# Performance work log

Hardware: AMD Instinct MI355X
Metric: run time of the kernel (lower is better)

Reference implementation:

```python
import jax, jax.numpy as jnp
import numpy as np

B, T, DIM, HEADS, DH = 4, 2048, 1024, 16, 64  # dh = dim // heads


def setup_inputs() -> dict:
    key = jax.random.key(0)
    k1, k2, k3 = jax.random.split(key, 3)
    x = jax.random.normal(k1, (B, T, DIM), dtype=jnp.float32)
    # nn.Linear weights, stored as [in, out] for x @ W convention
    W_qkv = jax.random.normal(k2, (DIM, 3 * HEADS * DH), dtype=jnp.float32) * (DIM ** -0.5)
    W_o = jax.random.normal(k3, (HEADS * DH, DIM), dtype=jnp.float32) * ((HEADS * DH) ** -0.5)
    return {"x": x, "W_qkv": W_qkv, "W_o": W_o}


def reference(x, W_qkv, W_o):
    b, t, _ = x.shape
    qkv = x @ W_qkv  # [b, t, 3*h*dh]
    # einops 'b t (d k h) -> k b h t d' with k=3, h=HEADS: fused axis splits as (dh, 3, h)
    qkv = qkv.reshape(b, t, DH, 3, HEADS)
    qkv = jnp.transpose(qkv, (3, 0, 4, 1, 2))  # [3, b, h, t, dh]
    q, k, v = qkv[0], qkv[1], qkv[2]
    scale = DH ** -0.5
    scores = jnp.einsum('bhid,bhjd->bhij', q, k) * scale  # [b, h, t, t]
    attn = jax.nn.softmax(scores, axis=-1)
    out = jnp.einsum('bhij,bhjd->bhid', attn, v)  # [b, h, t, dh]
    out = jnp.transpose(out, (0, 2, 1, 3)).reshape(b, t, HEADS * DH)  # 'b h t d -> b t (h d)'
    return out @ W_o
```

## Files before the change

kernel.cpp:

```cpp
#include <hip/hip_runtime.h>

typedef __bf16 bf16;
typedef __bf16 bf16x4 __attribute__((ext_vector_type(4)));
typedef __bf16 bf16x8 __attribute__((ext_vector_type(8)));
typedef float  f32x4  __attribute__((ext_vector_type(4)));
typedef unsigned int u32;
typedef unsigned int u32x2 __attribute__((ext_vector_type(2)));
typedef unsigned int u32x4 __attribute__((ext_vector_type(4)));

#define LOG2E 1.44269504088896340736f
#define EXP_SC (0.125f * LOG2E)

#if __has_builtin(__builtin_amdgcn_exp2f)
#define EXP2F(x) __builtin_amdgcn_exp2f(x)
#else
#define EXP2F(x) __builtin_exp2f(x)
#endif

__device__ __forceinline__ u32 pk_bf16(float lo, float hi) {
  u32 a = __float_as_uint(lo) + 0x8000u;
  u32 b = __float_as_uint(hi) + 0x8000u;
  return __builtin_amdgcn_perm(b, a, 0x07060302);
}
__device__ __forceinline__ unsigned short bf16r(float x) {
  return (unsigned short)((__float_as_uint(x) + 0x8000u) >> 16);
}

__device__ __forceinline__ void async_ld16(void* lds, const void* g) {
  __builtin_amdgcn_global_load_lds(
      (const __attribute__((address_space(1))) void*)(g),
      (__attribute__((address_space(3))) void*)(lds),
      16, 0, 0);
}

__global__ void convert_x(const float* __restrict__ x, bf16* __restrict__ xb) {
  int i = blockIdx.x * 256 + threadIdx.x;
  float4 v = ((const float4*)x)[i];
  u32x2 o = { pk_bf16(v.x, v.y), pk_bf16(v.z, v.w) };
  *(u32x2*)(xb + (size_t)i * 4) = o;
}

__global__ void prep_wqkv(const float* __restrict__ W, bf16* __restrict__ WT) {
  __shared__ float s[4 * 3072];
  const int k0 = blockIdx.x * 4;
  for (int i = threadIdx.x; i < 3072; i += 256) {
    int r = i / 768, c = (i - r * 768) * 4;
    *(float4*)(s + r * 3072 + c) = *(const float4*)(W + (size_t)(k0 + r) * 3072 + c);
  }
  __syncthreads();
  for (int n = threadIdx.x; n < 3072; n += 256) {
    int d = n & 63, h = (n >> 6) & 15, wch = n >> 10;
    int on = d * 48 + wch * 16 + h;
    u32x2 v = { pk_bf16(s[0 * 3072 + on], s[1 * 3072 + on]),
                pk_bf16(s[2 * 3072 + on], s[3 * 3072 + on]) };
    *(u32x2*)(WT + (size_t)n * 1024 + k0) = v;
  }
}

__global__ void prep_wo(const float* __restrict__ W, bf16* __restrict__ WT) {
  __shared__ float s[8 * 1024];
  const int k0 = blockIdx.x * 8;
  for (int i = threadIdx.x; i < 2048; i += 256) {
    int r = i >> 8, c = (i & 255) * 4;
    *(float4*)(s + r * 1024 + c) = *(const float4*)(W + (size_t)(k0 + r) * 1024 + c);
  }
  __syncthreads();
  for (int n = threadIdx.x; n < 1024; n += 256) {
    u32x4 v = { pk_bf16(s[0 * 1024 + n], s[1 * 1024 + n]),
                pk_bf16(s[2 * 1024 + n], s[3 * 1024 + n]),
                pk_bf16(s[4 * 1024 + n], s[5 * 1024 + n]),
                pk_bf16(s[6 * 1024 + n], s[7 * 1024 + n]) };
    *(u32x4*)(WT + (size_t)n * 1024 + k0) = v;
  }
}

template <int MODE>
__launch_bounds__(256, 2)
__global__ void gemm_bt(const bf16* __restrict__ A, const bf16* __restrict__ BT,
                        float* __restrict__ C, int N,
                        bf16* __restrict__ Qb, bf16* __restrict__ Kb, bf16* __restrict__ Vb) {
  constexpr int K = 1024;
  __shared__ bf16 sA[128 * 32];
  __shared__ bf16 sB[128 * 32];
  const int m0 = blockIdx.y * 128;
  const int n0 = blockIdx.x * 128;
  const int tid = threadIdx.x;
  const int lane = tid & 63;
  const int w = tid >> 6;
  const int wm = (w >> 1) * 64, wn = (w & 1) * 64;
  const int l15 = lane & 15, quad = lane >> 4;

  f32x4 acc[4][4];
  for (int i = 0; i < 4; i++)
    for (int j = 0; j < 4; j++) acc[i][j] = f32x4{0.f, 0.f, 0.f, 0.f};

  const int c0 = w * 128 + lane;
  const int c1 = c0 + 64;
  const int r0 = c0 >> 2, jg0 = (c0 & 3) ^ (r0 & 3);
  const int r1 = c1 >> 2, jg1 = (c1 & 3) ^ (r1 & 3);

  const bf16* gA0 = A  + (size_t)(m0 + r0) * K + jg0 * 8;
  const bf16* gA1 = A  + (size_t)(m0 + r1) * K + jg1 * 8;
  const bf16* gB0 = BT + (size_t)(n0 + r0) * K + jg0 * 8;
  const bf16* gB1 = BT + (size_t)(n0 + r1) * K + jg1 * 8;

  for (int k0 = 0; k0 < K; k0 += 32) {
    __syncthreads();
    async_ld16((void*)(sA + (w * 2) * 512),     gA0);
    async_ld16((void*)(sA + (w * 2 + 1) * 512), gA1);
    async_ld16((void*)(sB + (w * 2) * 512),     gB0);
    async_ld16((void*)(sB + (w * 2 + 1) * 512), gB1);
    gA0 += 32; gA1 += 32; gB0 += 32; gB1 += 32;
    __syncthreads();

    bf16x8 af[4], bfr[4];
    for (int ms = 0; ms < 4; ms++) {
      int r = wm + ms * 16 + l15;
      af[ms] = *(const bf16x8*)(sA + r * 32 + ((quad ^ (r & 3)) * 8));
    }
    for (int ns = 0; ns < 4; ns++) {
      int r = wn + ns * 16 + l15;
      bfr[ns] = *(const bf16x8*)(sB + r * 32 + ((quad ^ (r & 3)) * 8));
    }
    for (int ms = 0; ms < 4; ms++)
      for (int ns = 0; ns < 4; ns++)
        acc[ms][ns] = __builtin_amdgcn_mfma_f32_16x16x32_bf16(af[ms], bfr[ns], acc[ms][ns], 0, 0, 0);
  }

  if (MODE == 0) {
    for (int ms = 0; ms < 4; ms++)
      for (int ns = 0; ns < 4; ns++)
        for (int r = 0; r < 4; r++) {
          int row = m0 + wm + ms * 16 + quad * 4 + r;
          int col = n0 + wn + ns * 16 + l15;
          C[(size_t)row * N + col] = acc[ms][ns][r];
        }
  } else {
    for (int ms = 0; ms < 4; ms++)
      for (int ns = 0; ns < 4; ns++)
        for (int r = 0; r < 4; r++) {
          int row = m0 + wm + ms * 16 + quad * 4 + r;
          int col = n0 + wn + ns * 16 + l15;
          int b = row >> 11, t = row & 2047;
          int d = col & 63, h = (col >> 6) & 15, wch = col >> 10;
          bf16* dst = (wch == 0) ? Qb : (wch == 1) ? Kb : Vb;
          float v = acc[ms][ns][r] * ((wch == 0) ? EXP_SC : 1.0f);
          ((unsigned short*)dst)[(((size_t)(b * 16 + h)) * 2048 + t) * 64 + d] = bf16r(v);
        }
  }
}

__global__ void transpose_v(const bf16* __restrict__ V, bf16* __restrict__ VT) {
  __shared__ bf16 s[64 * 66];
  const int bh = blockIdx.y;
  const int t0 = blockIdx.x * 64;
  for (int i = threadIdx.x; i < 512; i += 256) {
    int t = i >> 3, dc = (i & 7) * 8;
    bf16x8 v = *(const bf16x8*)(V + ((size_t)bh * 2048 + t0 + t) * 64 + dc);
    for (int j = 0; j < 8; j++) s[t * 66 + dc + j] = v[j];
  }
  __syncthreads();
  for (int i = threadIdx.x; i < 512; i += 256) {
    int d = i >> 3, tc = (i & 7) * 8;
    bf16x8 v;
    for (int j = 0; j < 8; j++) {
      int kp = tc + j;
      int src = ((kp & 3) * 16) + (kp >> 2);
      v[j] = s[src * 66 + d];
    }
    *(bf16x8*)(VT + ((size_t)bh * 64 + d) * 2048 + t0 + tc) = v;
  }
}

__launch_bounds__(256, 2)
__global__ void attn_fwd(const bf16* __restrict__ Q, const bf16* __restrict__ K,
                         const bf16* __restrict__ VT, bf16* __restrict__ O) {
  __shared__ bf16 sK[64 * 64];
  __shared__ bf16 sV[64 * 64];
  __shared__ bf16 sP[4][32 * 64];
  const int bh = blockIdx.y;
  const int q0 = blockIdx.x * 128;
  const int tid = threadIdx.x;
  const int lane = tid & 63, w = tid >> 6;
  const int l15 = lane & 15, quad = lane >> 4;

  bf16x8 qf[2][2];
  for (int ms = 0; ms < 2; ms++)
    for (int kk = 0; kk < 2; kk++)
      qf[ms][kk] = *(const bf16x8*)(Q + ((size_t)bh * 2048 + q0 + w * 32 + ms * 16 + l15) * 64 + kk * 32 + quad * 8);

  f32x4 oa[2][4], lacc[2];
  for (int ms = 0; ms < 2; ms++) {
    for (int ds = 0; ds < 4; ds++) oa[ms][ds] = f32x4{0.f, 0.f, 0.f, 0.f};
    lacc[ms] = f32x4{0.f, 0.f, 0.f, 0.f};
  }
  bf16x8 onesf;
  for (int i = 0; i < 8; i++) onesf[i] = (bf16)1.0f;

  const int cA = w * 128 + lane;
  const int cB = cA + 64;
  const int rA = cA >> 3, jA = (cA & 7) ^ (rA & 7);
  const int rB = cB >> 3, jB = (cB & 7) ^ (rB & 7);
  const bf16* gKA = K  + ((size_t)bh * 2048 + rA) * 64 + jA * 8;
  const bf16* gKB = K  + ((size_t)bh * 2048 + rB) * 64 + jB * 8;
  const bf16* gVA = VT + ((size_t)bh * 64 + rA) * 2048 + jA * 8;
  const bf16* gVB = VT + ((size_t)bh * 64 + rB) * 2048 + jB * 8;

  int kvo[4][2], pfo[2][2], pwo[2][4];
  for (int ns = 0; ns < 4; ns++)
    for (int kk = 0; kk < 2; kk++) {
      int r = ns * 16 + l15;
      kvo[ns][kk] = r * 64 + (((kk * 4 + quad) ^ (r & 7)) * 8);
    }
  for (int ms = 0; ms < 2; ms++) {
    int r = ms * 16 + l15;
    for (int kk = 0; kk < 2; kk++)
      pfo[ms][kk] = r * 64 + (((kk * 4 + quad) ^ (r & 7)) * 8);
    for (int rr = 0; rr < 4; rr++) {
      int row = ms * 16 + quad * 4 + rr;
      pwo[ms][rr] = row * 64 + (((l15 >> 1) ^ (row & 7)) * 8) + (l15 & 1) * 4;
    }
  }

  for (int kt = 0; kt < 2048; kt += 64) {
    __syncthreads();
    async_ld16((void*)(sK + w * 1024),       gKA);
    async_ld16((void*)(sV + w * 1024),       gVA);
    async_ld16((void*)(sK + w * 1024 + 512), gKB);
    async_ld16((void*)(sV + w * 1024 + 512), gVB);
    gKA += 4096; gKB += 4096; gVA += 64; gVB += 64;
    __syncthreads();

    bf16x8 kf[4][2];
    for (int ns = 0; ns < 4; ns++)
      for (int kk = 0; kk < 2; kk++)
        kf[ns][kk] = *(const bf16x8*)(sK + kvo[ns][kk]);
    for (int ms = 0; ms < 2; ms++) {
      f32x4 s[4];
      for (int ns = 0; ns < 4; ns++) {
        f32x4 t = f32x4{0.f, 0.f, 0.f, 0.f};
        t = __builtin_amdgcn_mfma_f32_16x16x32_bf16(qf[ms][0], kf[ns][0], t, 0, 0, 0);
        t = __builtin_amdgcn_mfma_f32_16x16x32_bf16(qf[ms][1], kf[ns][1], t, 0, 0, 0);
        s[ns] = t;
      }
      for (int r = 0; r < 4; r++) {
        u32x2 pk = { pk_bf16(EXP2F(s[0][r]), EXP2F(s[1][r])),
                     pk_bf16(EXP2F(s[2][r]), EXP2F(s[3][r])) };
        *(u32x2*)(sP[w] + pwo[ms][r]) = pk;
      }
    }

    bf16x8 vf[4][2];
    for (int ds = 0; ds < 4; ds++)
      for (int kk = 0; kk < 2; kk++)
        vf[ds][kk] = *(const bf16x8*)(sV + kvo[ds][kk]);
    for (int ms = 0; ms < 2; ms++) {
      bf16x8 pf0 = *(const bf16x8*)(sP[w] + pfo[ms][0]);
      bf16x8 pf1 = *(const bf16x8*)(sP[w] + pfo[ms][1]);
      lacc[ms] = __builtin_amdgcn_mfma_f32_16x16x32_bf16(pf0, onesf, lacc[ms], 0, 0, 0);
      lacc[ms] = __builtin_amdgcn_mfma_f32_16x16x32_bf16(pf1, onesf, lacc[ms], 0, 0, 0);
      for (int ds = 0; ds < 4; ds++) {
        oa[ms][ds] = __builtin_amdgcn_mfma_f32_16x16x32_bf16(pf0, vf[ds][0], oa[ms][ds], 0, 0, 0);
        oa[ms][ds] = __builtin_amdgcn_mfma_f32_16x16x32_bf16(pf1, vf[ds][1], oa[ms][ds], 0, 0, 0);
      }
    }
  }

  const int b = bh >> 4, h = bh & 15;
  for (int ms = 0; ms < 2; ms++)
    for (int r = 0; r < 4; r++) {
      float inv = 1.0f / lacc[ms][r];
      int t = q0 + w * 32 + ms * 16 + quad * 4 + r;
      for (int ds = 0; ds < 4; ds++)
        ((unsigned short*)O)[((size_t)b * 2048 + t) * 1024 + h * 64 + ds * 16 + l15] =
            bf16r(oa[ms][ds][r] * inv);
    }
}

extern "C" void kernel_launch(void* const* d_in, const int* in_sizes, int n_in,
                              void* d_out, int out_size, void* d_ws, size_t ws_size,
                              hipStream_t stream) {
  const float* x    = (const float*)d_in[0];
  const float* Wqkv = (const float*)d_in[1];
  const float* Wo   = (const float*)d_in[2];
  float* out = (float*)d_out;
  char* ws = (char*)d_ws;

  bf16* wqkvT = (bf16*)(ws);
  bf16* woT   = (bf16*)(ws + 6291456);
  bf16* xb    = (bf16*)(ws + 8388608);
  bf16* Qb    = (bf16*)(ws + 25165824);
  bf16* Kb    = (bf16*)(ws + 41943040);
  bf16* Vb    = (bf16*)(ws + 58720256);
  bf16* VTb   = xb;
  bf16* AOb   = Vb;

  convert_x<<<8192, 256, 0, stream>>>(x, xb);
  prep_wqkv<<<256, 256, 0, stream>>>(Wqkv, wqkvT);
  prep_wo<<<128, 256, 0, stream>>>(Wo, woT);
  gemm_bt<1><<<dim3(24, 64), 256, 0, stream>>>(xb, wqkvT, nullptr, 3072, Qb, Kb, Vb);
  transpose_v<<<dim3(32, 64), 256, 0, stream>>>(Vb, VTb);
  attn_fwd<<<dim3(16, 64), 256, 0, stream>>>(Qb, Kb, VTb, AOb);
  gemm_bt<0><<<dim3(8, 64), 256, 0, stream>>>(AOb, woT, out, 1024, nullptr, nullptr, nullptr);
}
```

Baseline: 287.1 us.

## Merge prep kernels, deepen GEMM K-tile to 64, swap grid axes, use hardware bf16 convert

Merges the three fp32-to-bf16 prep kernels into one launch that dispatches on block index. The GEMM now stages 64-wide K tiles with an 8-way XOR swizzle, which halves the barrier count per K. Grid axes in the GEMMs and attention are swapped so consecutive blocks walk M or batch-head first, which changes L2 reuse of the weight and K/V tiles. The softmax packing uses the hardware cvt_pk_bf16 instruction when available, which reduces ALU work in the attention inner loop.

New measurement: 268.7 us. 1.07x faster.

```diff
diff --git a/kernel.cpp b/kernel.cpp
--- a/kernel.cpp
+++ b/kernel.cpp
@@ -1,6 +1,7 @@
 #include <hip/hip_runtime.h>
 
 typedef __bf16 bf16;
+typedef __bf16 bf16x2 __attribute__((ext_vector_type(2)));
 typedef __bf16 bf16x4 __attribute__((ext_vector_type(4)));
 typedef __bf16 bf16x8 __attribute__((ext_vector_type(8)));
 typedef float  f32x4  __attribute__((ext_vector_type(4)));
@@ -22,6 +23,14 @@
   u32 b = __float_as_uint(hi) + 0x8000u;
   return __builtin_amdgcn_perm(b, a, 0x07060302);
 }
+#if __has_builtin(__builtin_amdgcn_cvt_pk_bf16_f32)
+__device__ __forceinline__ u32 cvtpk(float lo, float hi) {
+  bf16x2 t = __builtin_amdgcn_cvt_pk_bf16_f32(lo, hi);
+  return __builtin_bit_cast(u32, t);
+}
+#else
+__device__ __forceinline__ u32 cvtpk(float lo, float hi) { return pk_bf16(lo, hi); }
+#endif
 __device__ __forceinline__ unsigned short bf16r(float x) {
   return (unsigned short)((__float_as_uint(x) + 0x8000u) >> 16);
 }
@@ -33,44 +42,45 @@
       16, 0, 0);
 }
 
-__global__ void convert_x(const float* __restrict__ x, bf16* __restrict__ xb) {
-  int i = blockIdx.x * 256 + threadIdx.x;
-  float4 v = ((const float4*)x)[i];
-  u32x2 o = { pk_bf16(v.x, v.y), pk_bf16(v.z, v.w) };
-  *(u32x2*)(xb + (size_t)i * 4) = o;
-}
-
-__global__ void prep_wqkv(const float* __restrict__ W, bf16* __restrict__ WT) {
-  __shared__ float s[4 * 3072];
-  const int k0 = blockIdx.x * 4;
-  for (int i = threadIdx.x; i < 3072; i += 256) {
-    int r = i / 768, c = (i - r * 768) * 4;
-    *(float4*)(s + r * 3072 + c) = *(const float4*)(W + (size_t)(k0 + r) * 3072 + c);
-  }
-  __syncthreads();
-  for (int n = threadIdx.x; n < 3072; n += 256) {
-    int d = n & 63, h = (n >> 6) & 15, wch = n >> 10;
-    int on = d * 48 + wch * 16 + h;
-    u32x2 v = { pk_bf16(s[0 * 3072 + on], s[1 * 3072 + on]),
-                pk_bf16(s[2 * 3072 + on], s[3 * 3072 + on]) };
-    *(u32x2*)(WT + (size_t)n * 1024 + k0) = v;
-  }
-}
-
-__global__ void prep_wo(const float* __restrict__ W, bf16* __restrict__ WT) {
-  __shared__ float s[8 * 1024];
-  const int k0 = blockIdx.x * 8;
-  for (int i = threadIdx.x; i < 2048; i += 256) {
-    int r = i >> 8, c = (i & 255) * 4;
-    *(float4*)(s + r * 1024 + c) = *(const float4*)(W + (size_t)(k0 + r) * 1024 + c);
-  }
-  __syncthreads();
-  for (int n = threadIdx.x; n < 1024; n += 256) {
-    u32x4 v = { pk_bf16(s[0 * 1024 + n], s[1 * 1024 + n]),
-                pk_bf16(s[2 * 1024 + n], s[3 * 1024 + n]),
-                pk_bf16(s[4 * 1024 + n], s[5 * 1024 + n]),
-                pk_bf16(s[6 * 1024 + n], s[7 * 1024 + n]) };
-    *(u32x4*)(WT + (size_t)n * 1024 + k0) = v;
+__global__ void prep_all(const float* __restrict__ x,    bf16* __restrict__ xb,
+                         const float* __restrict__ Wqkv, bf16* __restrict__ wqkvT,
+                         const float* __restrict__ Wo,   bf16* __restrict__ woT) {
+  __shared__ float s[12288];
+  const int bid = blockIdx.x;
+  const int tid = threadIdx.x;
+  if (bid < 8192) {
+    int i = bid * 256 + tid;
+    float4 v = ((const float4*)x)[i];
+    u32x2 o = { pk_bf16(v.x, v.y), pk_bf16(v.z, v.w) };
+    *(u32x2*)(xb + (size_t)i * 4) = o;
+  } else if (bid < 8448) {
+    const int k0 = (bid - 8192) * 4;
+    for (int i = tid; i < 3072; i += 256) {
+      int r = i / 768, c = (i - r * 768) * 4;
+      *(float4*)(s + r * 3072 + c) = *(const float4*)(Wqkv + (size_t)(k0 + r) * 3072 + c);
+    }
+    __syncthreads();
+    for (int n = tid; n < 3072; n += 256) {
+      int d = n & 63, h = (n >> 6) & 15, wch = n >> 10;
+      int on = d * 48 + wch * 16 + h;
+      u32x2 v = { pk_bf16(s[0 * 3072 + on], s[1 * 3072 + on]),
+                  pk_bf16(s[2 * 3072 + on], s[3 * 3072 + on]) };
+      *(u32x2*)(wqkvT + (size_t)n * 1024 + k0) = v;
+    }
+  } else {
+    const int k0 = (bid - 8448) * 8;
+    for (int i = tid; i < 2048; i += 256) {
+      int r = i >> 8, c = (i & 255) * 4;
+      *(float4*)(s + r * 1024 + c) = *(const float4*)(Wo + (size_t)(k0 + r) * 1024 + c);
+    }
+    __syncthreads();
+    for (int n = tid; n < 1024; n += 256) {
+      u32x4 v = { pk_bf16(s[0 * 1024 + n], s[1 * 1024 + n]),
+                  pk_bf16(s[2 * 1024 + n], s[3 * 1024 + n]),
+                  pk_bf16(s[4 * 1024 + n], s[5 * 1024 + n]),
+                  pk_bf16(s[6 * 1024 + n], s[7 * 1024 + n]) };
+      *(u32x4*)(woT + (size_t)n * 1024 + k0) = v;
+    }
   }
 }
 
@@ -80,10 +90,10 @@
                         float* __restrict__ C, int N,
                         bf16* __restrict__ Qb, bf16* __restrict__ Kb, bf16* __restrict__ Vb) {
   constexpr int K = 1024;
-  __shared__ bf16 sA[128 * 32];
-  __shared__ bf16 sB[128 * 32];
-  const int m0 = blockIdx.y * 128;
-  const int n0 = blockIdx.x * 128;
+  __shared__ bf16 sA[128 * 64];
+  __shared__ bf16 sB[128 * 64];
+  const int m0 = blockIdx.x * 128;
+  const int n0 = blockIdx.y * 128;
   const int tid = threadIdx.x;
   const int lane = tid & 63;
   const int w = tid >> 6;
@@ -94,37 +104,34 @@
   for (int i = 0; i < 4; i++)
     for (int j = 0; j < 4; j++) acc[i][j] = f32x4{0.f, 0.f, 0.f, 0.f};
 
-  const int c0 = w * 128 + lane;
-  const int c1 = c0 + 64;
-  const int r0 = c0 >> 2, jg0 = (c0 & 3) ^ (r0 & 3);
-  const int r1 = c1 >> 2, jg1 = (c1 & 3) ^ (r1 & 3);
-
-  const bf16* gA0 = A  + (size_t)(m0 + r0) * K + jg0 * 8;
-  const bf16* gA1 = A  + (size_t)(m0 + r1) * K + jg1 * 8;
-  const bf16* gB0 = BT + (size_t)(n0 + r0) * K + jg0 * 8;
-  const bf16* gB1 = BT + (size_t)(n0 + r1) * K + jg1 * 8;
-
-  for (int k0 = 0; k0 < K; k0 += 32) {
-    __syncthreads();
-    async_ld16((void*)(sA + (w * 2) * 512),     gA0);
-    async_ld16((void*)(sA + (w * 2 + 1) * 512), gA1);
-    async_ld16((void*)(sB + (w * 2) * 512),     gB0);
-    async_ld16((void*)(sB + (w * 2 + 1) * 512), gB1);
-    gA0 += 32; gA1 += 32; gB0 += 32; gB1 += 32;
-    __syncthreads();
-
-    bf16x8 af[4], bfr[4];
-    for (int ms = 0; ms < 4; ms++) {
-      int r = wm + ms * 16 + l15;
-      af[ms] = *(const bf16x8*)(sA + r * 32 + ((quad ^ (r & 3)) * 8));
-    }
-    for (int ns = 0; ns < 4; ns++) {
-      int r = wn + ns * 16 + l15;
-      bfr[ns] = *(const bf16x8*)(sB + r * 32 + ((quad ^ (r & 3)) * 8));
-    }
-    for (int ms = 0; ms < 4; ms++)
-      for (int ns = 0; ns < 4; ns++)
-        acc[ms][ns] = __builtin_amdgcn_mfma_f32_16x16x32_bf16(af[ms], bfr[ns], acc[ms][ns], 0, 0, 0);
+  const int rT = tid >> 3;
+  const int jT = (tid & 7) ^ (rT & 7);
+  const bf16* gA = A  + (size_t)(m0 + rT) * K + jT * 8;
+  const bf16* gB = BT + (size_t)(n0 + rT) * K + jT * 8;
+
+  for (int k0 = 0; k0 < K; k0 += 64) {
+    __syncthreads();
+    for (int i = 0; i < 4; i++) {
+      async_ld16((void*)(sA + (i * 256 + w * 64) * 8), gA + (size_t)i * 32 * K);
+      async_ld16((void*)(sB + (i * 256 + w * 64) * 8), gB + (size_t)i * 32 * K);
+    }
+    gA += 64; gB += 64;
+    __syncthreads();
+
+    for (int kk = 0; kk < 2; kk++) {
+      bf16x8 af[4], bfr[4];
+      for (int ms = 0; ms < 4; ms++) {
+        int r = wm + ms * 16 + l15;
+        af[ms] = *(const bf16x8*)(sA + r * 64 + (((kk * 4 + quad) ^ (r & 7)) * 8));
+      }
+      for (int ns = 0; ns < 4; ns++) {
+        int r = wn + ns * 16 + l15;
+        bfr[ns] = *(const bf16x8*)(sB + r * 64 + (((kk * 4 + quad) ^ (r & 7)) * 8));
+      }
+      for (int ms = 0; ms < 4; ms++)
+        for (int ns = 0; ns < 4; ns++)
+          acc[ms][ns] = __builtin_amdgcn_mfma_f32_16x16x32_bf16(af[ms], bfr[ns], acc[ms][ns], 0, 0, 0);
+    }
   }
 
   if (MODE == 0) {
@@ -178,8 +185,8 @@
   __shared__ bf16 sK[64 * 64];
   __shared__ bf16 sV[64 * 64];
   __shared__ bf16 sP[4][32 * 64];
-  const int bh = blockIdx.y;
-  const int q0 = blockIdx.x * 128;
+  const int bh = blockIdx.x;
+  const int q0 = blockIdx.y * 128;
   const int tid = threadIdx.x;
   const int lane = tid & 63, w = tid >> 6;
   const int l15 = lane & 15, quad = lane >> 4;
@@ -244,8 +251,8 @@
         s[ns] = t;
       }
       for (int r = 0; r < 4; r++) {
-        u32x2 pk = { pk_bf16(EXP2F(s[0][r]), EXP2F(s[1][r])),
-                     pk_bf16(EXP2F(s[2][r]), EXP2F(s[3][r])) };
+        u32x2 pk = { cvtpk(EXP2F(s[0][r]), EXP2F(s[1][r])),
+                     cvtpk(EXP2F(s[2][r]), EXP2F(s[3][r])) };
         *(u32x2*)(sP[w] + pwo[ms][r]) = pk;
       }
     }
@@ -295,11 +302,9 @@
   bf16* VTb   = xb;
   bf16* AOb   = Vb;
 
-  convert_x<<<8192, 256, 0, stream>>>(x, xb);
-  prep_wqkv<<<256, 256, 0, stream>>>(Wqkv, wqkvT);
-  prep_wo<<<128, 256, 0, stream>>>(Wo, woT);
-  gemm_bt<1><<<dim3(24, 64), 256, 0, stream>>>(xb, wqkvT, nullptr, 3072, Qb, Kb, Vb);
+  prep_all<<<8576, 256, 0, stream>>>(x, xb, Wqkv, wqkvT, Wo, woT);
+  gemm_bt<1><<<dim3(64, 24), 256, 0, stream>>>(xb, wqkvT, nullptr, 3072, Qb, Kb, Vb);
   transpose_v<<<dim3(32, 64), 256, 0, stream>>>(Vb, VTb);
-  attn_fwd<<<dim3(16, 64), 256, 0, stream>>>(Qb, Kb, VTb, AOb);
-  gemm_bt<0><<<dim3(8, 64), 256, 0, stream>>>(AOb, woT, out, 1024, nullptr, nullptr, nullptr);
-}
+  attn_fwd<<<dim3(64, 16), 256, 0, stream>>>(Qb, Kb, VTb, AOb);
+  gemm_bt<0><<<dim3(64, 8), 256, 0, stream>>>(AOb, woT, out, 1024, nullptr, nullptr, nullptr);
+}
```
